# Kernel optimization log

Hardware: AMD Instinct MI355X
Metric: run time of the kernel (lower is better)

## Reference

```python
import jax, jax.numpy as jnp
import numpy as np

DIM = 512
NUM_HEADS = 8
HEAD_DIM = DIM // NUM_HEADS
SCALE = HEAD_DIM ** -0.5


def setup_inputs() -> dict:
    key = jax.random.key(0)
    ks = jax.random.split(key, 6)
    B, N = 2, 4096
    x = jax.random.normal(ks[0], (B, N, DIM), dtype=jnp.float32)
    # xavier_uniform for qkv [3*dim, dim] and proj [dim, dim] (torch Linear weight layout [out,in])
    lim_qkv = float(np.sqrt(6.0 / (3 * DIM + DIM)))
    w_qkv = jax.random.uniform(ks[1], (3 * DIM, DIM), minval=-lim_qkv, maxval=lim_qkv, dtype=jnp.float32)
    lim_p = float(np.sqrt(6.0 / (DIM + DIM)))
    w_proj = jax.random.uniform(ks[2], (DIM, DIM), minval=-lim_p, maxval=lim_p, dtype=jnp.float32)
    b_proj = jnp.zeros((DIM,), dtype=jnp.float32)
    ln_gamma = jnp.ones((DIM,), dtype=jnp.float32)
    ln_beta = jnp.zeros((DIM,), dtype=jnp.float32)
    return {"x": x, "w_qkv": w_qkv, "w_proj": w_proj, "b_proj": b_proj,
            "ln_gamma": ln_gamma, "ln_beta": ln_beta}


def _attention(x, w_qkv, w_proj, b_proj, ln_gamma, ln_beta):
    B, N, C = x.shape
    qkv = jnp.einsum('bnc,dc->bnd', x, w_qkv)              # [B,N,3C]
    qkv = qkv.reshape(B, N, 3, NUM_HEADS, HEAD_DIM)
    qkv = jnp.transpose(qkv, (2, 0, 3, 1, 4))              # [3,B,H,N,Dh]
    q, k, v = qkv[0], qkv[1], qkv[2]
    attn = jnp.einsum('bhnd,bhmd->bhnm', q, k) * SCALE     # [B,H,N,N]
    attn = jax.nn.softmax(attn, axis=-1)
    # dropout is identity in eval mode
    out = jnp.einsum('bhnm,bhmd->bhnd', attn, v)           # [B,H,N,Dh]
    out = jnp.transpose(out, (0, 2, 1, 3)).reshape(B, N, C)
    out = jnp.einsum('bnc,dc->bnd', out, w_proj) + b_proj
    y = x + out
    mean = jnp.mean(y, axis=-1, keepdims=True)
    var = jnp.var(y, axis=-1, keepdims=True)
    return (y - mean) / jnp.sqrt(var + 1e-5) * ln_gamma + ln_beta


def reference(x, w_qkv, w_proj, b_proj, ln_gamma, ln_beta):
    return _attention(x, w_qkv, w_proj, b_proj, ln_gamma, ln_beta)
```

## Files before the change

kernel.cpp:

```cpp
#include <hip/hip_runtime.h>
#include <hip/hip_bf16.h>

#define SEQ    4096
#define CDIM   512
#define NHEADS 8
#define HDIM   64
#define QSCALE 0.18033688f

typedef __attribute__((ext_vector_type(4))) float f32x4;
typedef __attribute__((ext_vector_type(8))) short bf16x8;

__device__ __forceinline__ int swz(int row, int col) {
    int b = (row << 7) + (col << 1);
    b ^= (row & 7) << 4;
    return b >> 1;
}

__device__ __forceinline__ short f2bf(float f) {
    union { __hip_bfloat16 h; short s; } u;
    u.h = __float2bfloat16(f);
    return u.s;
}

__device__ __forceinline__ void gl16(const void* g, void* l) {
    __builtin_amdgcn_global_load_lds(
        (const __attribute__((address_space(1))) unsigned int*)g,
        (__attribute__((address_space(3))) unsigned int*)l,
        16, 0, 0);
}

__global__ __launch_bounds__(256) void cvt_k(
    const float* __restrict__ a, short* __restrict__ o, int n4)
{
    int i = blockIdx.x * 256 + threadIdx.x;
    const int stride = gridDim.x * 256;
    for (; i < n4; i += stride) {
        float4 v = ((const float4*)a)[i];
        short4 r;
        r.x = f2bf(v.x); r.y = f2bf(v.y); r.z = f2bf(v.z); r.w = f2bf(v.w);
        ((short4*)o)[i] = r;
    }
}

__global__ __launch_bounds__(256) void qkv_gemm_k(
    const short* __restrict__ xb, const short* __restrict__ wb,
    short* __restrict__ qb, short* __restrict__ kb, short* __restrict__ vtb)
{
    __shared__ alignas(16) short As[2][128 * 64];
    __shared__ alignas(16) short Bs[2][128 * 64];
    const int tid  = threadIdx.x;
    const int lane = tid & 63;
    const int l15  = lane & 15;
    const int lg   = lane >> 4;
    const int wv   = tid >> 6;
    const int wy   = wv >> 1, wx = wv & 1;
    const int m0 = blockIdx.x * 128;
    const int n0 = blockIdx.y * 128;

    const f32x4 fzero = {0.f, 0.f, 0.f, 0.f};
    f32x4 acc[4][4];
    #pragma unroll
    for (int i = 0; i < 4; ++i)
        #pragma unroll
        for (int j = 0; j < 4; ++j)
            acc[i][j] = fzero;

    const int row0 = wv * 8 + (lane >> 3);
    const int cb   = ((lane & 7) ^ (lane >> 3)) << 4;
    const char* agp = (const char*)xb + (size_t)(m0 + row0) * 1024 + cb;
    const char* bgp = (const char*)wb + (size_t)(n0 + row0) * 1024 + cb;
    char* al0 = (char*)&As[0][0] + wv * 1024;
    char* al1 = (char*)&As[1][0] + wv * 1024;
    char* bl0 = (char*)&Bs[0][0] + wv * 1024;
    char* bl1 = (char*)&Bs[1][0] + wv * 1024;

    #define QSTAGE(al, bl, kofs) do {                                  \
        _Pragma("unroll")                                              \
        for (int i_ = 0; i_ < 4; ++i_) {                               \
            gl16(agp + (kofs) + i_ * 32768, (al) + i_ * 4096);         \
            gl16(bgp + (kofs) + i_ * 32768, (bl) + i_ * 4096);         \
        } } while (0)

    QSTAGE(al0, bl0, 0);

    int cur = 0;
    for (int k0 = 0; k0 < CDIM; k0 += 64) {
        asm volatile("s_waitcnt vmcnt(0)" ::: "memory");
        __syncthreads();
        if (k0 + 64 < CDIM) {
            if (cur == 0) QSTAGE(al1, bl1, (k0 + 64) * 2);
            else          QSTAGE(al0, bl0, (k0 + 64) * 2);
        }
        const short* Ac = cur ? &As[1][0] : &As[0][0];
        const short* Bc = cur ? &Bs[1][0] : &Bs[0][0];

        #pragma unroll
        for (int ks = 0; ks < 2; ++ks) {
            bf16x8 afr[4], bfr[4];
            #pragma unroll
            for (int i = 0; i < 4; ++i) {
                afr[i] = *(const bf16x8*)(&Ac[swz(wy * 64 + i * 16 + l15, ks * 32 + lg * 8)]);
                bfr[i] = *(const bf16x8*)(&Bc[swz(wx * 64 + i * 16 + l15, ks * 32 + lg * 8)]);
            }
            #pragma unroll
            for (int i = 0; i < 4; ++i)
                #pragma unroll
                for (int j = 0; j < 4; ++j)
                    acc[i][j] = __builtin_amdgcn_mfma_f32_16x16x32_bf16(afr[i], bfr[j], acc[i][j], 0, 0, 0);
        }
        cur ^= 1;
    }
    #undef QSTAGE

    #pragma unroll
    for (int j = 0; j < 4; ++j) {
        const int d = n0 + wx * 64 + j * 16 + l15;
        const int s = d >> 9;
        const int h = (d >> 6) & 7;
        const int e = d & 63;
        #pragma unroll
        for (int i = 0; i < 4; ++i) {
            #pragma unroll
            for (int r = 0; r < 4; ++r) {
                const int m  = m0 + wy * 64 + i * 16 + lg * 4 + r;
                const int bb = m >> 12;
                const int n  = m & (SEQ - 1);
                const int bh = bb * NHEADS + h;
                const float v = acc[i][j][r];
                if (s == 0) {
                    qb[(((size_t)bh * SEQ + n) << 6) + e] = f2bf(v * QSCALE);
                } else if (s == 1) {
                    kb[(((size_t)bh * SEQ + n) << 6) + e] = f2bf(v);
                } else {
                    const int c  = n & 63;
                    const int cp = (c & 0x23) | ((c & 0x0C) << 1) | ((c & 0x10) >> 2);
                    vtb[((size_t)bh << 18) + ((size_t)(n >> 6) << 12) + (e << 6) + cp] = f2bf(v);
                }
            }
        }
    }
}

__global__ __launch_bounds__(512) void attn_k(
    const short* __restrict__ qb, const short* __restrict__ kb, const short* __restrict__ vtb,
    short* __restrict__ ob)
{
    __shared__ alignas(16) char smem[65536];
    const int tid  = threadIdx.x;
    const int lane = tid & 63;
    const int l15  = lane & 15;
    const int lg   = lane >> 4;
    const int wv   = (tid >> 6) & 3;
    const int wg   = tid >> 8;
    const int lin  = blockIdx.x;
    const int bh   = lin & 15;
    const int q0   = (lin >> 4) << 7;
    const int b    = bh >> 3, h = bh & 7;
    const size_t base = (size_t)bh * SEQ * HDIM;

    bf16x8 qf[2][2];
    #pragma unroll
    for (int qi = 0; qi < 2; ++qi) {
        const short* qp = qb + base + (size_t)(q0 + wv * 32 + qi * 16 + l15) * HDIM + lg * 8;
        qf[qi][0] = *(const bf16x8*)(qp);
        qf[qi][1] = *(const bf16x8*)(qp + 32);
    }

    const f32x4 fzero = {0.f, 0.f, 0.f, 0.f};
    f32x4 acc[2][4];
    f32x4 lacc[2];
    #pragma unroll
    for (int qi = 0; qi < 2; ++qi) {
        lacc[qi] = fzero;
        #pragma unroll
        for (int di = 0; di < 4; ++di) acc[qi][di] = fzero;
    }

    bf16x8 ones;
    #pragma unroll
    for (int e = 0; e < 8; ++e) ones[e] = (short)0x3F80;

    const int t0  = wv * 128 + lane;
    const int cbs = ((t0 & 7) ^ ((t0 >> 3) & 7)) << 4;
    const int ghb = wg * 262144;
    const char* kgp = (const char*)(kb + base) + ghb + (((t0 >> 3) << 7) + cbs);
    const char* vgp = (const char*)(vtb + ((size_t)bh << 18)) + ghb + (((t0 >> 3) << 7) + cbs);
    char* const gbase = smem + wg * 32768;
    char* kl0 = gbase + wv * 2048;
    char* kl1 = gbase + 8192  + wv * 2048;
    char* vl0 = gbase + 16384 + wv * 2048;
    char* vl1 = gbase + 16384 + 8192 + wv * 2048;

    #define STAGE(kl, vl, gofs) do {                               \
        _Pragma("unroll")                                          \
        for (int i_ = 0; i_ < 2; ++i_) {                           \
            gl16(kgp + (gofs) + i_ * 1024, (kl) + i_ * 1024);      \
            gl16(vgp + (gofs) + i_ * 1024, (vl) + i_ * 1024);      \
        } } while (0)

    STAGE(kl0, vl0, 0);

    int cur = 0;
    for (int kt = 0; kt < SEQ / 2; kt += 64) {
        asm volatile("s_waitcnt vmcnt(0)" ::: "memory");
        __syncthreads();

        if (kt + 64 < SEQ / 2) {
            if (cur == 0) STAGE(kl1, vl1, (kt + 64) * 128);
            else          STAGE(kl0, vl0, (kt + 64) * 128);
        }

        const short* Kc = (const short*)(gbase + cur * 8192);
        const short* Vc = (const short*)(gbase + 16384 + cur * 8192);

        f32x4 s[2][4];
        #pragma unroll
        for (int qi = 0; qi < 2; ++qi)
            #pragma unroll
            for (int ni = 0; ni < 4; ++ni) s[qi][ni] = fzero;
        __builtin_amdgcn_s_setprio(1);
        #pragma unroll
        for (int kk = 0; kk < 2; ++kk)
            #pragma unroll
            for (int ni = 0; ni < 4; ++ni) {
                bf16x8 kf = *(const bf16x8*)(&Kc[swz(ni * 16 + l15, kk * 32 + lg * 8)]);
                s[0][ni] = __builtin_amdgcn_mfma_f32_16x16x32_bf16(kf, qf[0][kk], s[0][ni], 0, 0, 0);
                s[1][ni] = __builtin_amdgcn_mfma_f32_16x16x32_bf16(kf, qf[1][kk], s[1][ni], 0, 0, 0);
            }
        __builtin_amdgcn_s_setprio(0);

        #pragma unroll
        for (int ks = 0; ks < 2; ++ks) {
            bf16x8 pa0, pa1;
            #pragma unroll
            for (int e = 0; e < 8; ++e) {
                pa0[e] = f2bf(__builtin_amdgcn_exp2f(s[0][ks * 2 + (e >> 2)][e & 3]));
                pa1[e] = f2bf(__builtin_amdgcn_exp2f(s[1][ks * 2 + (e >> 2)][e & 3]));
            }
            __builtin_amdgcn_s_setprio(1);
            lacc[0] = __builtin_amdgcn_mfma_f32_16x16x32_bf16(pa0, ones, lacc[0], 0, 0, 0);
            lacc[1] = __builtin_amdgcn_mfma_f32_16x16x32_bf16(pa1, ones, lacc[1], 0, 0, 0);
            #pragma unroll
            for (int di = 0; di < 4; ++di) {
                bf16x8 vfr = *(const bf16x8*)(&Vc[swz(di * 16 + l15, ks * 32 + lg * 8)]);
                acc[0][di] = __builtin_amdgcn_mfma_f32_16x16x32_bf16(pa0, vfr, acc[0][di], 0, 0, 0);
                acc[1][di] = __builtin_amdgcn_mfma_f32_16x16x32_bf16(pa1, vfr, acc[1][di], 0, 0, 0);
            }
            __builtin_amdgcn_s_setprio(0);
        }

        cur ^= 1;
    }
    #undef STAGE

    __syncthreads();
    float* xch = (float*)smem;
    const int xi = (wv * 64 + lane) * 44;
    if (wg == 1) {
        #pragma unroll
        for (int qi = 0; qi < 2; ++qi) {
            #pragma unroll
            for (int di = 0; di < 4; ++di)
                *(f32x4*)(xch + xi + qi * 16 + di * 4) = acc[qi][di];
            *(f32x4*)(xch + xi + 32 + qi * 4) = lacc[qi];
        }
    }
    __syncthreads();
    if (wg == 0) {
        #pragma unroll
        for (int qi = 0; qi < 2; ++qi) {
            #pragma unroll
            for (int di = 0; di < 4; ++di)
                acc[qi][di] += *(const f32x4*)(xch + xi + qi * 16 + di * 4);
            lacc[qi] += *(const f32x4*)(xch + xi + 32 + qi * 4);
        }
        #pragma unroll
        for (int qi = 0; qi < 2; ++qi) {
            float inv[4];
            #pragma unroll
            for (int r = 0; r < 4; ++r) inv[r] = 1.0f / lacc[qi][r];
            #pragma unroll
            for (int di = 0; di < 4; ++di) {
                const int e = di * 16 + l15;
                #pragma unroll
                for (int r = 0; r < 4; ++r) {
                    const int qn = q0 + wv * 32 + qi * 16 + lg * 4 + r;
                    ob[((size_t)(b * SEQ + qn) << 9) + h * 64 + e] = f2bf(acc[qi][di][r] * inv[r]);
                }
            }
        }
    }
}

__global__ __launch_bounds__(256) void proj_k(
    const short* __restrict__ ao, const short* __restrict__ wpb,
    const float* __restrict__ bp, const float* __restrict__ x,
    float* __restrict__ y)
{
    __shared__ alignas(16) short As[2][128 * 64];
    __shared__ alignas(16) short Bs[2][128 * 64];
    const int tid  = threadIdx.x;
    const int lane = tid & 63;
    const int l15  = lane & 15;
    const int lg   = lane >> 4;
    const int wv   = tid >> 6;
    const int wy   = wv >> 1, wx = wv & 1;
    const int m0 = blockIdx.x * 128;
    const int n0 = blockIdx.y * 128;

    const f32x4 fzero = {0.f, 0.f, 0.f, 0.f};
    f32x4 acc[4][4];
    #pragma unroll
    for (int i = 0; i < 4; ++i)
        #pragma unroll
        for (int j = 0; j < 4; ++j)
            acc[i][j] = fzero;

    const int row0 = wv * 8 + (lane >> 3);
    const int cb   = ((lane & 7) ^ (lane >> 3)) << 4;
    const char* agp = (const char*)ao  + (size_t)(m0 + row0) * 1024 + cb;
    const char* bgp = (const char*)wpb + (size_t)(n0 + row0) * 1024 + cb;
    char* al0 = (char*)&As[0][0] + wv * 1024;
    char* al1 = (char*)&As[1][0] + wv * 1024;
    char* bl0 = (char*)&Bs[0][0] + wv * 1024;
    char* bl1 = (char*)&Bs[1][0] + wv * 1024;

    #define PSTAGE(al, bl, kofs) do {                                  \
        _Pragma("unroll")                                              \
        for (int i_ = 0; i_ < 4; ++i_) {                               \
            gl16(agp + (kofs) + i_ * 32768, (al) + i_ * 4096);         \
            gl16(bgp + (kofs) + i_ * 32768, (bl) + i_ * 4096);         \
        } } while (0)

    PSTAGE(al0, bl0, 0);

    int cur = 0;
    for (int k0 = 0; k0 < CDIM; k0 += 64) {
        asm volatile("s_waitcnt vmcnt(0)" ::: "memory");
        __syncthreads();
        if (k0 + 64 < CDIM) {
            if (cur == 0) PSTAGE(al1, bl1, (k0 + 64) * 2);
            else          PSTAGE(al0, bl0, (k0 + 64) * 2);
        }
        const short* Ac = cur ? &As[1][0] : &As[0][0];
        const short* Bc = cur ? &Bs[1][0] : &Bs[0][0];

        #pragma unroll
        for (int ks = 0; ks < 2; ++ks) {
            bf16x8 afr[4], bfr[4];
            #pragma unroll
            for (int i = 0; i < 4; ++i) {
                afr[i] = *(const bf16x8*)(&Ac[swz(wy * 64 + i * 16 + l15, ks * 32 + lg * 8)]);
                bfr[i] = *(const bf16x8*)(&Bc[swz(wx * 64 + i * 16 + l15, ks * 32 + lg * 8)]);
            }
            #pragma unroll
            for (int i = 0; i < 4; ++i)
                #pragma unroll
                for (int j = 0; j < 4; ++j)
                    acc[i][j] = __builtin_amdgcn_mfma_f32_16x16x32_bf16(afr[i], bfr[j], acc[i][j], 0, 0, 0);
        }
        cur ^= 1;
    }
    #undef PSTAGE

    #pragma unroll
    for (int i = 0; i < 4; ++i) {
        #pragma unroll
        for (int j = 0; j < 4; ++j) {
            const int d = n0 + wx * 64 + j * 16 + l15;
            #pragma unroll
            for (int r = 0; r < 4; ++r) {
                const int m = m0 + wy * 64 + i * 16 + lg * 4 + r;
                const size_t idx = (size_t)m * CDIM + d;
                y[idx] = acc[i][j][r] + bp[d] + x[idx];
            }
        }
    }
}

__global__ __launch_bounds__(256) void ln_k(
    float* __restrict__ y, const float* __restrict__ gm, const float* __restrict__ bt)
{
    const int lane = threadIdx.x & 63;
    const int row  = blockIdx.x * 4 + (threadIdx.x >> 6);
    float* p = y + (size_t)row * CDIM;
    float4 a = *(const float4*)(p + lane * 4);
    float4 b = *(const float4*)(p + 256 + lane * 4);
    float s = a.x + a.y + a.z + a.w + b.x + b.y + b.z + b.w;
    float q = a.x * a.x + a.y * a.y + a.z * a.z + a.w * a.w
            + b.x * b.x + b.y * b.y + b.z * b.z + b.w * b.w;
    #pragma unroll
    for (int mm = 1; mm < 64; mm <<= 1) {
        s += __shfl_xor(s, mm, 64);
        q += __shfl_xor(q, mm, 64);
    }
    const float mean = s * (1.0f / CDIM);
    const float var  = q * (1.0f / CDIM) - mean * mean;
    const float inv  = rsqrtf(var + 1e-5f);
    float4 g0 = *(const float4*)(gm + lane * 4);
    float4 g1 = *(const float4*)(gm + 256 + lane * 4);
    float4 t0 = *(const float4*)(bt + lane * 4);
    float4 t1 = *(const float4*)(bt + 256 + lane * 4);
    float4 r0, r1;
    r0.x = (a.x - mean) * inv * g0.x + t0.x;
    r0.y = (a.y - mean) * inv * g0.y + t0.y;
    r0.z = (a.z - mean) * inv * g0.z + t0.z;
    r0.w = (a.w - mean) * inv * g0.w + t0.w;
    r1.x = (b.x - mean) * inv * g1.x + t1.x;
    r1.y = (b.y - mean) * inv * g1.y + t1.y;
    r1.z = (b.z - mean) * inv * g1.z + t1.z;
    r1.w = (b.w - mean) * inv * g1.w + t1.w;
    *(float4*)(p + lane * 4) = r0;
    *(float4*)(p + 256 + lane * 4) = r1;
}

extern "C" void kernel_launch(void* const* d_in, const int* in_sizes, int n_in,
                              void* d_out, int out_size, void* d_ws, size_t ws_size,
                              hipStream_t stream)
{
    const float* x      = (const float*)d_in[0];
    const float* w_qkv  = (const float*)d_in[1];
    const float* w_proj = (const float*)d_in[2];
    const float* b_proj = (const float*)d_in[3];
    const float* gamma  = (const float*)d_in[4];
    const float* beta   = (const float*)d_in[5];
    float* out = (float*)d_out;

    const size_t qkv_elems = (size_t)16 * SEQ * HDIM;
    short* qb    = (short*)d_ws;
    short* kb    = qb + qkv_elems;
    short* vtb   = kb + qkv_elems;
    short* ob    = vtb + qkv_elems;
    short* xb    = ob;
    short* wqkvb = ob + qkv_elems;
    short* wpb   = qb;

    cvt_k     <<<dim3(1024),   256, 0, stream>>>(x, xb, (2 * SEQ * CDIM) / 4);
    cvt_k     <<<dim3(256),    256, 0, stream>>>(w_qkv, wqkvb, (3 * CDIM * CDIM) / 4);
    qkv_gemm_k<<<dim3(64, 12), 256, 0, stream>>>(xb, wqkvb, qb, kb, vtb);
    attn_k    <<<dim3(512),    512, 0, stream>>>(qb, kb, vtb, ob);
    cvt_k     <<<dim3(256),    256, 0, stream>>>(w_proj, wpb, (CDIM * CDIM) / 4);
    proj_k    <<<dim3(64, 4),  256, 0, stream>>>(ob, wpb, b_proj, x, out);
    ln_k      <<<dim3(2048),   256, 0, stream>>>(out, gamma, beta);
}
```

Before: 122.0 us.

## Software-pipeline attention loop: overlap next tile's exp with current PV MFMAs

Restructures the attention inner loop into a software pipeline. The softmax exponentials for tile T are computed while the PV MFMAs for tile T-1 run, using ping-pong probability registers, a triple-buffered V tile and a double-buffered K tile in a larger LDS allocation. The loop is unrolled by six to rotate buffers statically, and the s_setprio hints are removed. The aim is to hide the transcendental/VALU cost behind matrix-core work, at the price of more LDS (80KB per block), more registers, and a launch-bounds occupancy hint.

```diff
diff --git a/kernel.cpp b/kernel.cpp
--- a/kernel.cpp
+++ b/kernel.cpp
@@ -141,11 +141,11 @@
     }
 }
 
-__global__ __launch_bounds__(512) void attn_k(
+__global__ __launch_bounds__(512, 4) void attn_k(
     const short* __restrict__ qb, const short* __restrict__ kb, const short* __restrict__ vtb,
     short* __restrict__ ob)
 {
-    __shared__ alignas(16) char smem[65536];
+    __shared__ alignas(16) char smem[81920];
     const int tid  = threadIdx.x;
     const int lane = tid & 63;
     const int l15  = lane & 15;
@@ -185,72 +185,111 @@
     const int ghb = wg * 262144;
     const char* kgp = (const char*)(kb + base) + ghb + (((t0 >> 3) << 7) + cbs);
     const char* vgp = (const char*)(vtb + ((size_t)bh << 18)) + ghb + (((t0 >> 3) << 7) + cbs);
-    char* const gbase = smem + wg * 32768;
-    char* kl0 = gbase + wv * 2048;
-    char* kl1 = gbase + 8192  + wv * 2048;
-    char* vl0 = gbase + 16384 + wv * 2048;
-    char* vl1 = gbase + 16384 + 8192 + wv * 2048;
-
-    #define STAGE(kl, vl, gofs) do {                               \
-        _Pragma("unroll")                                          \
-        for (int i_ = 0; i_ < 2; ++i_) {                           \
-            gl16(kgp + (gofs) + i_ * 1024, (kl) + i_ * 1024);      \
-            gl16(vgp + (gofs) + i_ * 1024, (vl) + i_ * 1024);      \
+    char* const gb = smem + wg * 40960;
+    char* K0p = gb +     0 + wv * 2048;  const short* Kr0 = (const short*)(gb);
+    char* K1p = gb +  8192 + wv * 2048;  const short* Kr1 = (const short*)(gb + 8192);
+    char* V0p = gb + 16384 + wv * 2048;  const short* Vr0 = (const short*)(gb + 16384);
+    char* V1p = gb + 24576 + wv * 2048;  const short* Vr1 = (const short*)(gb + 24576);
+    char* V2p = gb + 32768 + wv * 2048;  const short* Vr2 = (const short*)(gb + 32768);
+
+    bf16x8 paA[2][2], paB[2][2];
+
+    #define STAGE(klp, vlp, TI) do {                                       \
+        _Pragma("unroll")                                                  \
+        for (int i_ = 0; i_ < 2; ++i_) {                                   \
+            gl16(kgp + (TI) * 8192 + i_ * 1024, (klp) + i_ * 1024);        \
+            gl16(vgp + (TI) * 8192 + i_ * 1024, (vlp) + i_ * 1024);        \
         } } while (0)
 
-    STAGE(kl0, vl0, 0);
-
-    int cur = 0;
-    for (int kt = 0; kt < SEQ / 2; kt += 64) {
-        asm volatile("s_waitcnt vmcnt(0)" ::: "memory");
-        __syncthreads();
-
-        if (kt + 64 < SEQ / 2) {
-            if (cur == 0) STAGE(kl1, vl1, (kt + 64) * 128);
-            else          STAGE(kl0, vl0, (kt + 64) * 128);
-        }
-
-        const short* Kc = (const short*)(gbase + cur * 8192);
-        const short* Vc = (const short*)(gbase + 16384 + cur * 8192);
-
+    #define BODY(TILE, KRD, VPR, KSTP, VSTP, PAP, PAN, DOSTG) do {         \
+        asm volatile("s_waitcnt vmcnt(0)" ::: "memory");                   \
+        __syncthreads();                                                   \
+        if (DOSTG) { STAGE(KSTP, VSTP, (TILE) + 1); }                      \
+        f32x4 s[2][4];                                                     \
+        _Pragma("unroll")                                                  \
+        for (int qi = 0; qi < 2; ++qi)                                     \
+            _Pragma("unroll")                                              \
+            for (int ni = 0; ni < 4; ++ni) s[qi][ni] = fzero;              \
+        _Pragma("unroll")                                                  \
+        for (int kk = 0; kk < 2; ++kk)                                     \
+            _Pragma("unroll")                                              \
+            for (int ni = 0; ni < 4; ++ni) {                               \
+                bf16x8 kf = *(const bf16x8*)(&(KRD)[swz(ni * 16 + l15, kk * 32 + lg * 8)]); \
+                s[0][ni] = __builtin_amdgcn_mfma_f32_16x16x32_bf16(kf, qf[0][kk], s[0][ni], 0, 0, 0); \
+                s[1][ni] = __builtin_amdgcn_mfma_f32_16x16x32_bf16(kf, qf[1][kk], s[1][ni], 0, 0, 0); \
+            }                                                              \
+        _Pragma("unroll")                                                  \
+        for (int dd = 0; dd < 4; ++dd) {                                   \
+            bf16x8 v0 = *(const bf16x8*)(&(VPR)[swz(dd * 16 + l15, lg * 8)]);      \
+            bf16x8 v1 = *(const bf16x8*)(&(VPR)[swz(dd * 16 + l15, 32 + lg * 8)]); \
+            acc[0][dd] = __builtin_amdgcn_mfma_f32_16x16x32_bf16(PAP[0][0], v0, acc[0][dd], 0, 0, 0); \
+            acc[0][dd] = __builtin_amdgcn_mfma_f32_16x16x32_bf16(PAP[0][1], v1, acc[0][dd], 0, 0, 0); \
+            acc[1][dd] = __builtin_amdgcn_mfma_f32_16x16x32_bf16(PAP[1][0], v0, acc[1][dd], 0, 0, 0); \
+            acc[1][dd] = __builtin_amdgcn_mfma_f32_16x16x32_bf16(PAP[1][1], v1, acc[1][dd], 0, 0, 0); \
+            _Pragma("unroll")                                              \
+            for (int e = 0; e < 8; ++e)                                    \
+                PAN[dd >> 1][dd & 1][e] = f2bf(__builtin_amdgcn_exp2f(     \
+                    s[dd >> 1][(dd & 1) * 2 + (e >> 2)][e & 3]));          \
+        }                                                                  \
+        lacc[0] = __builtin_amdgcn_mfma_f32_16x16x32_bf16(PAP[0][0], ones, lacc[0], 0, 0, 0); \
+        lacc[0] = __builtin_amdgcn_mfma_f32_16x16x32_bf16(PAP[0][1], ones, lacc[0], 0, 0, 0); \
+        lacc[1] = __builtin_amdgcn_mfma_f32_16x16x32_bf16(PAP[1][0], ones, lacc[1], 0, 0, 0); \
+        lacc[1] = __builtin_amdgcn_mfma_f32_16x16x32_bf16(PAP[1][1], ones, lacc[1], 0, 0, 0); \
+    } while (0)
+
+    STAGE(K0p, V0p, 0);
+    asm volatile("s_waitcnt vmcnt(0)" ::: "memory");
+    __syncthreads();
+    STAGE(K1p, V1p, 1);
+    {
         f32x4 s[2][4];
         #pragma unroll
         for (int qi = 0; qi < 2; ++qi)
             #pragma unroll
             for (int ni = 0; ni < 4; ++ni) s[qi][ni] = fzero;
-        __builtin_amdgcn_s_setprio(1);
         #pragma unroll
         for (int kk = 0; kk < 2; ++kk)
             #pragma unroll
             for (int ni = 0; ni < 4; ++ni) {
-                bf16x8 kf = *(const bf16x8*)(&Kc[swz(ni * 16 + l15, kk * 32 + lg * 8)]);
+                bf16x8 kf = *(const bf16x8*)(&Kr0[swz(ni * 16 + l15, kk * 32 + lg * 8)]);
                 s[0][ni] = __builtin_amdgcn_mfma_f32_16x16x32_bf16(kf, qf[0][kk], s[0][ni], 0, 0, 0);
                 s[1][ni] = __builtin_amdgcn_mfma_f32_16x16x32_bf16(kf, qf[1][kk], s[1][ni], 0, 0, 0);
             }
-        __builtin_amdgcn_s_setprio(0);
-
-        #pragma unroll
-        for (int ks = 0; ks < 2; ++ks) {
-            bf16x8 pa0, pa1;
-            #pragma unroll
-            for (int e = 0; e < 8; ++e) {
-                pa0[e] = f2bf(__builtin_amdgcn_exp2f(s[0][ks * 2 + (e >> 2)][e & 3]));
-                pa1[e] = f2bf(__builtin_amdgcn_exp2f(s[1][ks * 2 + (e >> 2)][e & 3]));
-            }
-            __builtin_amdgcn_s_setprio(1);
-            lacc[0] = __builtin_amdgcn_mfma_f32_16x16x32_bf16(pa0, ones, lacc[0], 0, 0, 0);
-            lacc[1] = __builtin_amdgcn_mfma_f32_16x16x32_bf16(pa1, ones, lacc[1], 0, 0, 0);
-            #pragma unroll
-            for (int di = 0; di < 4; ++di) {
-                bf16x8 vfr = *(const bf16x8*)(&Vc[swz(di * 16 + l15, ks * 32 + lg * 8)]);
-                acc[0][di] = __builtin_amdgcn_mfma_f32_16x16x32_bf16(pa0, vfr, acc[0][di], 0, 0, 0);
-                acc[1][di] = __builtin_amdgcn_mfma_f32_16x16x32_bf16(pa1, vfr, acc[1][di], 0, 0, 0);
-            }
-            __builtin_amdgcn_s_setprio(0);
-        }
-
-        cur ^= 1;
-    }
+        #pragma unroll
+        for (int qi = 0; qi < 2; ++qi)
+            #pragma unroll
+            for (int ni = 0; ni < 4; ++ni)
+                #pragma unroll
+                for (int r = 0; r < 4; ++r)
+                    paA[qi][ni >> 1][(ni & 1) * 4 + r] =
+                        f2bf(__builtin_amdgcn_exp2f(s[qi][ni][r]));
+    }
+
+    for (int i = 0; i < 5; ++i) {
+        const int T = 6 * i + 1;
+        BODY(T,     Kr1, Vr0, K0p, V2p, paA, paB, 1);
+        BODY(T + 1, Kr0, Vr1, K1p, V0p, paB, paA, 1);
+        BODY(T + 2, Kr1, Vr2, K0p, V1p, paA, paB, 1);
+        BODY(T + 3, Kr0, Vr0, K1p, V2p, paB, paA, 1);
+        BODY(T + 4, Kr1, Vr1, K0p, V0p, paA, paB, 1);
+        BODY(T + 5, Kr0, Vr2, K1p, V1p, paB, paA, 1);
+    }
+    BODY(31, Kr1, Vr0, K0p, V2p, paA, paB, 0);
+
+    #pragma unroll
+    for (int dd = 0; dd < 4; ++dd) {
+        bf16x8 v0 = *(const bf16x8*)(&Vr1[swz(dd * 16 + l15, lg * 8)]);
+        bf16x8 v1 = *(const bf16x8*)(&Vr1[swz(dd * 16 + l15, 32 + lg * 8)]);
+        acc[0][dd] = __builtin_amdgcn_mfma_f32_16x16x32_bf16(paB[0][0], v0, acc[0][dd], 0, 0, 0);
+        acc[0][dd] = __builtin_amdgcn_mfma_f32_16x16x32_bf16(paB[0][1], v1, acc[0][dd], 0, 0, 0);
+        acc[1][dd] = __builtin_amdgcn_mfma_f32_16x16x32_bf16(paB[1][0], v0, acc[1][dd], 0, 0, 0);
+        acc[1][dd] = __builtin_amdgcn_mfma_f32_16x16x32_bf16(paB[1][1], v1, acc[1][dd], 0, 0, 0);
+    }
+    lacc[0] = __builtin_amdgcn_mfma_f32_16x16x32_bf16(paB[0][0], ones, lacc[0], 0, 0, 0);
+    lacc[0] = __builtin_amdgcn_mfma_f32_16x16x32_bf16(paB[0][1], ones, lacc[0], 0, 0, 0);
+    lacc[1] = __builtin_amdgcn_mfma_f32_16x16x32_bf16(paB[1][0], ones, lacc[1], 0, 0, 0);
+    lacc[1] = __builtin_amdgcn_mfma_f32_16x16x32_bf16(paB[1][1], ones, lacc[1], 0, 0, 0);
+    #undef BODY
     #undef STAGE
 
     __syncthreads();
```

Measured after the change: 288.5 us. +136.5%, slower.
